# Performance work log

Measured on AMD Instinct MI355X. Metric: run time of the kernel, lower is better.

Reference implementation:

```python
import jax, jax.numpy as jnp
import numpy as np

DN = ('NCHW', 'OIHW', 'NCHW')

def _conv(x, w, b, pad):
    y = jax.lax.conv_general_dilated(x, w, (1, 1), pad, dimension_numbers=DN)
    return y + b[None, :, None, None]

def setup_inputs() -> dict:
    key = jax.random.key(0)
    ks = jax.random.split(key, 8)
    B, C, H, W = 8, 256, 64, 64
    C8 = C // 8
    return {
        'x': jax.random.normal(ks[0], (B, C, H, W), jnp.float32),
        'wq': jax.random.normal(ks[1], (C8, C, 1, 3), jnp.float32) * 0.02,
        'bq': jax.random.normal(ks[2], (C8,), jnp.float32) * 0.02,
        'wk': jax.random.normal(ks[3], (C8, C, 3, 1), jnp.float32) * 0.02,
        'bk': jax.random.normal(ks[4], (C8,), jnp.float32) * 0.02,
        'wv': jax.random.normal(ks[5], (C, C, 1, 1), jnp.float32) * 0.02,
        'bv': jax.random.normal(ks[6], (C,), jnp.float32) * 0.02,
        'gamma': jax.random.normal(ks[7], (1,), jnp.float32),
    }

def reference(x, wq, bq, wk, bk, wv, bv, gamma):
    B, C, H, W = x.shape
    N = H * W
    # q: (1,3) kernel, pad (0,1); k: (3,1) kernel, pad (1,0); v: 1x1
    q = _conv(x, wq, bq, [(0, 0), (1, 1)]).reshape(B, -1, N)  # B, C/8, N
    k = _conv(x, wk, bk, [(1, 1), (0, 0)]).reshape(B, -1, N)  # B, C/8, N
    v = _conv(x, wv, bv, [(0, 0), (0, 0)]).reshape(B, C, N)   # B, C, N
    affinity = jnp.einsum('bci,bcj->bij', q, k)               # B, N, N
    affinity = jax.nn.softmax(affinity, axis=-1)
    # weights = v @ affinity^T  ->  (B, C, N)
    weights = jnp.einsum('bcj,bij->bci', v, affinity).reshape(B, C, H, W)
    return gamma[0] * weights + x
```

## Files before the change

### kernel.cpp

```cpp
#include <hip/hip_runtime.h>
#include <math.h>

#define BB 8
#define CCH 256
#define C8 32
#define NN 4096
#define LOG2E 1.44269504f

typedef unsigned short us;
typedef __attribute__((ext_vector_type(8))) short bf16x8;
typedef __attribute__((ext_vector_type(4))) float f32x4;
typedef __attribute__((ext_vector_type(16))) float f32x16;

static __device__ __forceinline__ us f2bf(float f) {
  union { float f; unsigned u; } v; v.f = f;
  unsigned r = v.u + 0x7fffu + ((v.u >> 16) & 1u);
  return (us)(r >> 16);
}
static __device__ __forceinline__ us f2bf_rhu(float f) {
  return (us)((__float_as_uint(f) + 0x8000u) >> 16);
}
template <int CTRL>
static __device__ __forceinline__ float dpp_mv(float x) {
  return __int_as_float(
      __builtin_amdgcn_update_dpp(0, __float_as_int(x), CTRL, 0xF, 0xF, false));
}
static __device__ __forceinline__ float rowsum16(float t) {
  t += dpp_mv<0x121>(t);
  t += dpp_mv<0x122>(t);
  t += dpp_mv<0x124>(t);
  t += dpp_mv<0x128>(t);
  return t;
}

__global__ __launch_bounds__(256) void prep_kernel(
    const float* __restrict__ x, const float* __restrict__ wq,
    const float* __restrict__ wk, const float* __restrict__ wv,
    us* __restrict__ xT, us* __restrict__ wqc, us* __restrict__ wkc,
    us* __restrict__ wvb) {
  __shared__ __align__(16) us lt[64 * 68];
  int bid = blockIdx.x;
  int tid = threadIdx.x;
  if (bid < 2048) {
    int b = bid >> 8, cb = (bid >> 6) & 3, nb = bid & 63;
    const float* xb = x + (((size_t)(b * 256 + cb * 64)) << 12);
    int nl = tid & 63, ch = tid >> 6;
#pragma unroll
    for (int p = 0; p < 16; p++) {
      int c = p * 4 + ch;
      lt[nl * 68 + c] = f2bf(xb[((size_t)c << 12) + (nb * 64 + nl)]);
    }
    __syncthreads();
    us* xTb = xT + (((size_t)b << 12) + nb * 64) * 256 + cb * 64;
    int cw = tid & 7, nr0 = tid >> 3;
#pragma unroll
    for (int p2 = 0; p2 < 2; p2++) {
      int nr = p2 * 32 + nr0;
      uint2 lo = *(const uint2*)&lt[nr * 68 + cw * 8];
      uint2 hi = *(const uint2*)&lt[nr * 68 + cw * 8 + 4];
      *(uint4*)&xTb[(size_t)nr * 256 + cw * 8] = make_uint4(lo.x, lo.y, hi.x, hi.y);
    }
  } else {
    int idx = (bid - 2048) * 256 + tid;
    if (idx < 24576) {
      int oc = idx / 768, r = idx % 768, t = r >> 8, ic = r & 255;
      wqc[idx] = f2bf(wq[(oc * 256 + ic) * 3 + t] * LOG2E);
    } else if (idx < 49152) {
      int j = idx - 24576;
      int oc = j / 768, r = j % 768, t = r >> 8, ic = r & 255;
      wkc[j] = f2bf(wk[(oc * 256 + ic) * 3 + t]);
    } else if (idx < 114688) {
      int j = idx - 49152;
      wvb[j] = f2bf(wv[j]);
    }
  }
}

__global__ __launch_bounds__(256) void conv_kernel(
    const us* __restrict__ xT, const us* __restrict__ wqc,
    const us* __restrict__ wkc, const float* __restrict__ bq,
    const float* __restrict__ bk, const us* __restrict__ wvb,
    const float* __restrict__ bv, us* __restrict__ qT, us* __restrict__ kT,
    us* __restrict__ vblk) {
  int tid = threadIdx.x, lane = tid & 63, w = tid >> 6;
  int l15 = lane & 15, quad = lane >> 4;
  if (blockIdx.x < 512) {
    int bid = blockIdx.x;
    int b = bid & 7, rt = bid >> 3;
    int n0 = rt * 64, y = rt;
    bool isq = (w < 2);
    int m0 = (w & 1) * 16;
    const us* wc = isq ? wqc : wkc;
    const us* xTb = xT + (((size_t)b << 12) * 256);
    f32x4 acc[4];
#pragma unroll
    for (int nt = 0; nt < 4; nt++) acc[nt] = (f32x4){0.f, 0.f, 0.f, 0.f};
#pragma unroll
    for (int t = 0; t < 3; t++) {
      bool killT = (!isq) && ((t == 0 && y == 0) || (t == 2 && y == 63));
      if (!killT) {
        int dn = isq ? (t - 1) : (t - 1) * 64;
#pragma unroll
        for (int k8 = 0; k8 < 8; k8++) {
          int kloc = t * 256 + k8 * 32 + quad * 8;
          bf16x8 af = *(const bf16x8*)(wc + (size_t)(m0 + l15) * 768 + kloc);
          int ic = k8 * 32 + quad * 8;
#pragma unroll
          for (int nt = 0; nt < 4; nt++) {
            int nl = nt * 16 + l15;
            int ns = n0 + nl + dn;
            ns = ns < 0 ? 0 : (ns > 4095 ? 4095 : ns);
            bf16x8 bf = *(const bf16x8*)(xTb + (size_t)ns * 256 + ic);
            if (isq && ((t == 0 && nl == 0) || (t == 2 && nl == 63)))
              bf = (bf16x8){0, 0, 0, 0, 0, 0, 0, 0};
            acc[nt] = __builtin_amdgcn_mfma_f32_16x16x32_bf16(af, bf, acc[nt], 0, 0, 0);
          }
        }
      }
    }
    const float* bias = isq ? bq : bk;
    float bsc = isq ? LOG2E : 1.0f;
    us* outp = (isq ? qT : kT) + (((size_t)b << 12) * 32);
    float b0 = bias[m0 + quad * 4 + 0] * bsc;
    float b1 = bias[m0 + quad * 4 + 1] * bsc;
    float b2 = bias[m0 + quad * 4 + 2] * bsc;
    float b3 = bias[m0 + quad * 4 + 3] * bsc;
#pragma unroll
    for (int nt = 0; nt < 4; nt++) {
      int n = n0 + nt * 16 + l15;
      unsigned lo = (unsigned)f2bf(acc[nt][0] + b0) | ((unsigned)f2bf(acc[nt][1] + b1) << 16);
      unsigned hi = (unsigned)f2bf(acc[nt][2] + b2) | ((unsigned)f2bf(acc[nt][3] + b3) << 16);
      *(uint2*)(outp + (size_t)n * 32 + m0 + quad * 4) = make_uint2(lo, hi);
    }
  } else {
    int bid = blockIdx.x - 512;
    int b = bid & 7, nt0 = bid >> 3;
    int n0 = nt0 * 64;
    const us* xTb = xT + (((size_t)b << 12) * 256);
    f32x4 acc[4][4];
#pragma unroll
    for (int ct = 0; ct < 4; ct++)
#pragma unroll
      for (int nt = 0; nt < 4; nt++) acc[ct][nt] = (f32x4){0.f, 0.f, 0.f, 0.f};
#pragma unroll
    for (int kk = 0; kk < 8; kk++) {
      bf16x8 bfr[4];
#pragma unroll
      for (int nt = 0; nt < 4; nt++)
        bfr[nt] = *(const bf16x8*)(xTb + (size_t)(n0 + nt * 16 + l15) * 256 + kk * 32 + quad * 8);
#pragma unroll
      for (int ct = 0; ct < 4; ct++) {
        bf16x8 wf = *(const bf16x8*)(wvb + (size_t)(w * 64 + ct * 16 + l15) * 256 + kk * 32 + quad * 8);
#pragma unroll
        for (int nt = 0; nt < 4; nt++)
          acc[ct][nt] = __builtin_amdgcn_mfma_f32_16x16x32_bf16(bfr[nt], wf, acc[ct][nt], 0, 0, 0);
      }
    }
    us* vb = vblk + ((size_t)b << 20);
#pragma unroll
    for (int ct = 0; ct < 4; ct++) {
      int oc = w * 64 + ct * 16 + l15;
      float bvv = bv[oc];
#pragma unroll
      for (int nt = 0; nt < 4; nt++) {
        unsigned lo = (unsigned)f2bf(acc[ct][nt][0] + bvv) | ((unsigned)f2bf(acc[ct][nt][1] + bvv) << 16);
        unsigned hi = (unsigned)f2bf(acc[ct][nt][2] + bvv) | ((unsigned)f2bf(acc[ct][nt][3] + bvv) << 16);
        *(uint2*)(vb + ((size_t)((n0 >> 4) + nt) * 256 + oc) * 16 + quad * 4) = make_uint2(lo, hi);
      }
    }
  }
}

__global__ __launch_bounds__(512, 4) void attn_kernel(
    const float* __restrict__ x, const us* __restrict__ qT,
    const us* __restrict__ kT, const us* __restrict__ vblk,
    const float* __restrict__ gamma_p, float* __restrict__ out) {
  __shared__ __align__(16) us pb[2][64 * 136];
  __shared__ float lpart[2][64];

  int tid = threadIdx.x, lane = tid & 63, w = tid >> 6;
  int l15 = lane & 15, quad = lane >> 4;
  int l31 = lane & 31, h32 = lane >> 5;
  int tw = w & 3, jh = w >> 2;

  int bid = blockIdx.x;
  int b = bid & 7, i0 = (bid >> 3) * 64;

  const us* qTb = qT + (((size_t)b << 12) * 32);
  const us* kTb = kT + (((size_t)b << 12) * 32);
  const us* vbb = vblk + ((size_t)b << 20);

  bf16x8 qf = *(const bf16x8*)(qTb + (size_t)(i0 + tw * 16 + l15) * 32 + quad * 8);

  float lr[4] = {0.f, 0.f, 0.f, 0.f};
  f32x16 o[2];
#pragma unroll
  for (int it = 0; it < 2; it++)
#pragma unroll
    for (int rg = 0; rg < 16; rg++) o[it][rg] = 0.f;

  int bu = 0;
  for (int jt = 0; jt < 32; jt++) {
    int j0 = jt * 128;
    bf16x8 kf[4];
#pragma unroll
    for (int j2 = 0; j2 < 4; j2++)
      kf[j2] = *(const bf16x8*)(kTb + (size_t)(j0 + jh * 64 + j2 * 16 + l15) * 32 + quad * 8);
    bf16x8 vf[8];
#pragma unroll
    for (int ks = 0; ks < 8; ks++)
      vf[ks] = *(const bf16x8*)(vbb + ((size_t)((j0 >> 4) + ks) * 256 + w * 32 + l31) * 16 + h32 * 8);
    f32x4 s[4];
#pragma unroll
    for (int j2 = 0; j2 < 4; j2++)
      s[j2] = __builtin_amdgcn_mfma_f32_16x16x32_bf16(qf, kf[j2], (f32x4){0.f, 0.f, 0.f, 0.f}, 0, 0, 0);
    us* pw = &pb[bu][(tw * 16 + quad * 4) * 136 + jh * 64 + l15];
#pragma unroll
    for (int j2 = 0; j2 < 4; j2++)
#pragma unroll
      for (int r = 0; r < 4; r++) {
        float p = __builtin_amdgcn_exp2f(s[j2][r]);
        lr[r] += p;
        pw[r * 136 + j2 * 16] = f2bf_rhu(p);
      }
    __syncthreads();
#pragma unroll
    for (int ks = 0; ks < 8; ks++) {
      bf16x8 pf0 = *(const bf16x8*)&pb[bu][(size_t)l31 * 136 + ks * 16 + h32 * 8];
      bf16x8 pf1 = *(const bf16x8*)&pb[bu][(size_t)(32 + l31) * 136 + ks * 16 + h32 * 8];
      o[0] = __builtin_amdgcn_mfma_f32_32x32x16_bf16(vf[ks], pf0, o[0], 0, 0, 0);
      o[1] = __builtin_amdgcn_mfma_f32_32x32x16_bf16(vf[ks], pf1, o[1], 0, 0, 0);
    }
    bu ^= 1;
  }

  float ls[4];
#pragma unroll
  for (int r = 0; r < 4; r++) ls[r] = rowsum16(lr[r]);
  if (l15 == 0) {
#pragma unroll
    for (int r = 0; r < 4; r++) lpart[jh][tw * 16 + quad * 4 + r] = ls[r];
  }
  __syncthreads();
  float g = gamma_p[0];
  const float* xb = x + ((size_t)b << 20);
  float* ob = out + ((size_t)b << 20);
  float gl[2];
#pragma unroll
  for (int it = 0; it < 2; it++) {
    int i = it * 32 + l31;
    gl[it] = g / (lpart[0][i] + lpart[1][i]);
  }
#pragma unroll
  for (int it = 0; it < 2; it++) {
    int i = i0 + it * 32 + l31;
#pragma unroll
    for (int rg = 0; rg < 16; rg++) {
      int c = w * 32 + ((rg & 3) + 8 * (rg >> 2) + 4 * h32);
      size_t idx = ((size_t)c << 12) + i;
      ob[idx] = o[it][rg] * gl[it] + xb[idx];
    }
  }
}

extern "C" void kernel_launch(void* const* d_in, const int* in_sizes, int n_in,
                              void* d_out, int out_size, void* d_ws, size_t ws_size,
                              hipStream_t stream) {
  const float* x = (const float*)d_in[0];
  const float* wq = (const float*)d_in[1];
  const float* bq = (const float*)d_in[2];
  const float* wk = (const float*)d_in[3];
  const float* bk = (const float*)d_in[4];
  const float* wv = (const float*)d_in[5];
  const float* bv = (const float*)d_in[6];
  const float* gamma = (const float*)d_in[7];
  float* out = (float*)d_out;

  us* xT = (us*)d_ws;
  us* qT = xT + (size_t)8388608;
  us* kT = qT + (size_t)1048576;
  us* vblk = kT + (size_t)1048576;
  us* wqc = vblk + (size_t)8388608;
  us* wkc = wqc + (size_t)24576;
  us* wvb = wkc + (size_t)24576;

  prep_kernel<<<2496, 256, 0, stream>>>(x, wq, wk, wv, xT, wqc, wkc, wvb);
  conv_kernel<<<1024, 256, 0, stream>>>(xT, wqc, wkc, bq, bk, wvb, bv, qT, kT, vblk);
  attn_kernel<<<512, 512, 0, stream>>>(x, qT, kT, vblk, gamma, out);
}
```

Baseline: 236.7 us.

## Keep softmax probabilities in registers via permlane32 swap instead of LDS

Restructures the attention kernel so each wave computes a transposed 32x32 score tile (K·Q) with 32x32x16 MFMA. It then rearranges the exp'd probabilities between lane halves with permlane32_swap so they can feed the PV MFMA directly as the B operand. This removes the LDS probability buffer, the per-tile __syncthreads and the cross-wave rowsum reduction. Blocks shrink to 256 threads, each wave owning 32 queries by 128 channels, and the next K tile is prefetched. The cost is that each wave redoes QK for its half of the channels, so score compute is duplicated, and V loads per wave increase.

```diff
diff --git a/kernel.cpp b/kernel.cpp
--- a/kernel.cpp
+++ b/kernel.cpp
@@ -17,21 +17,29 @@
   unsigned r = v.u + 0x7fffu + ((v.u >> 16) & 1u);
   return (us)(r >> 16);
 }
-static __device__ __forceinline__ us f2bf_rhu(float f) {
-  return (us)((__float_as_uint(f) + 0x8000u) >> 16);
-}
-template <int CTRL>
-static __device__ __forceinline__ float dpp_mv(float x) {
-  return __int_as_float(
-      __builtin_amdgcn_update_dpp(0, __float_as_int(x), CTRL, 0xF, 0xF, false));
-}
-static __device__ __forceinline__ float rowsum16(float t) {
-  t += dpp_mv<0x121>(t);
-  t += dpp_mv<0x122>(t);
-  t += dpp_mv<0x124>(t);
-  t += dpp_mv<0x128>(t);
-  return t;
-}
+static __device__ __forceinline__ unsigned pk_rhu(float a, float b) {
+  unsigned ua = (__float_as_uint(a) + 0x8000u) >> 16;
+  unsigned ub = (__float_as_uint(b) + 0x8000u) & 0xffff0000u;
+  return ua | ub;
+}
+
+#if __has_builtin(__builtin_amdgcn_permlane32_swap)
+static __device__ __forceinline__ void lane32_swap(unsigned& hi, unsigned& lo) {
+  auto r = __builtin_amdgcn_permlane32_swap((int)hi, (int)lo, false, false);
+  hi = (unsigned)r[0];
+  lo = (unsigned)r[1];
+}
+#else
+static __device__ __forceinline__ void lane32_swap(unsigned& hi, unsigned& lo) {
+  unsigned ph = (unsigned)__shfl_xor((int)hi, 32);
+  unsigned pl = (unsigned)__shfl_xor((int)lo, 32);
+  bool up = (threadIdx.x & 32) != 0;
+  unsigned nh = up ? hi : pl;
+  unsigned nl = up ? ph : lo;
+  hi = nh;
+  lo = nl;
+}
+#endif
 
 __global__ __launch_bounds__(256) void prep_kernel(
     const float* __restrict__ x, const float* __restrict__ wq,
@@ -171,94 +179,91 @@
   }
 }
 
-__global__ __launch_bounds__(512, 4) void attn_kernel(
+__global__ __launch_bounds__(256, 2) void attn_kernel(
     const float* __restrict__ x, const us* __restrict__ qT,
     const us* __restrict__ kT, const us* __restrict__ vblk,
     const float* __restrict__ gamma_p, float* __restrict__ out) {
-  __shared__ __align__(16) us pb[2][64 * 136];
-  __shared__ float lpart[2][64];
-
-  int tid = threadIdx.x, lane = tid & 63, w = tid >> 6;
-  int l15 = lane & 15, quad = lane >> 4;
+  int tid = threadIdx.x, lane = tid & 63;
+  int w = tid >> 6;
   int l31 = lane & 31, h32 = lane >> 5;
-  int tw = w & 3, jh = w >> 2;
+  int chalf = w & 1, ihalf = w >> 1;
 
   int bid = blockIdx.x;
-  int b = bid & 7, i0 = (bid >> 3) * 64;
+  int b = bid & 7, i0 = (bid >> 3) * 64 + ihalf * 32;
+  int c0 = chalf * 128;
 
   const us* qTb = qT + (((size_t)b << 12) * 32);
   const us* kTb = kT + (((size_t)b << 12) * 32);
   const us* vbb = vblk + ((size_t)b << 20);
 
-  bf16x8 qf = *(const bf16x8*)(qTb + (size_t)(i0 + tw * 16 + l15) * 32 + quad * 8);
-
-  float lr[4] = {0.f, 0.f, 0.f, 0.f};
-  f32x16 o[2];
-#pragma unroll
-  for (int it = 0; it < 2; it++)
-#pragma unroll
-    for (int rg = 0; rg < 16; rg++) o[it][rg] = 0.f;
-
-  int bu = 0;
-  for (int jt = 0; jt < 32; jt++) {
-    int j0 = jt * 128;
-    bf16x8 kf[4];
-#pragma unroll
-    for (int j2 = 0; j2 < 4; j2++)
-      kf[j2] = *(const bf16x8*)(kTb + (size_t)(j0 + jh * 64 + j2 * 16 + l15) * 32 + quad * 8);
-    bf16x8 vf[8];
-#pragma unroll
-    for (int ks = 0; ks < 8; ks++)
-      vf[ks] = *(const bf16x8*)(vbb + ((size_t)((j0 >> 4) + ks) * 256 + w * 32 + l31) * 16 + h32 * 8);
-    f32x4 s[4];
-#pragma unroll
-    for (int j2 = 0; j2 < 4; j2++)
-      s[j2] = __builtin_amdgcn_mfma_f32_16x16x32_bf16(qf, kf[j2], (f32x4){0.f, 0.f, 0.f, 0.f}, 0, 0, 0);
-    us* pw = &pb[bu][(tw * 16 + quad * 4) * 136 + jh * 64 + l15];
-#pragma unroll
-    for (int j2 = 0; j2 < 4; j2++)
-#pragma unroll
-      for (int r = 0; r < 4; r++) {
-        float p = __builtin_amdgcn_exp2f(s[j2][r]);
-        lr[r] += p;
-        pw[r * 136 + j2 * 16] = f2bf_rhu(p);
-      }
-    __syncthreads();
-#pragma unroll
-    for (int ks = 0; ks < 8; ks++) {
-      bf16x8 pf0 = *(const bf16x8*)&pb[bu][(size_t)l31 * 136 + ks * 16 + h32 * 8];
-      bf16x8 pf1 = *(const bf16x8*)&pb[bu][(size_t)(32 + l31) * 136 + ks * 16 + h32 * 8];
-      o[0] = __builtin_amdgcn_mfma_f32_32x32x16_bf16(vf[ks], pf0, o[0], 0, 0, 0);
-      o[1] = __builtin_amdgcn_mfma_f32_32x32x16_bf16(vf[ks], pf1, o[1], 0, 0, 0);
-    }
-    bu ^= 1;
-  }
-
-  float ls[4];
-#pragma unroll
-  for (int r = 0; r < 4; r++) ls[r] = rowsum16(lr[r]);
-  if (l15 == 0) {
-#pragma unroll
-    for (int r = 0; r < 4; r++) lpart[jh][tw * 16 + quad * 4 + r] = ls[r];
-  }
-  __syncthreads();
-  float g = gamma_p[0];
+  bf16x8 qf0 = *(const bf16x8*)(qTb + (size_t)(i0 + l31) * 32 + h32 * 8);
+  bf16x8 qf1 = *(const bf16x8*)(qTb + (size_t)(i0 + l31) * 32 + 16 + h32 * 8);
+
+  float lsum = 0.f;
+  f32x16 o[4];
+#pragma unroll
+  for (int ct = 0; ct < 4; ct++)
+#pragma unroll
+    for (int rg = 0; rg < 16; rg++) o[ct][rg] = 0.f;
+
+  bf16x8 kf0 = *(const bf16x8*)(kTb + (size_t)l31 * 32 + h32 * 8);
+  bf16x8 kf1 = *(const bf16x8*)(kTb + (size_t)l31 * 32 + 16 + h32 * 8);
+
+  for (int jt = 0; jt < 128; jt++) {
+    int j0 = jt * 32;
+    bf16x8 vf[4][2];
+#pragma unroll
+    for (int ct = 0; ct < 4; ct++)
+#pragma unroll
+      for (int win = 0; win < 2; win++)
+        vf[ct][win] = *(const bf16x8*)(vbb + ((size_t)((j0 >> 4) + win) * 256 + c0 + ct * 32 + l31) * 16 + h32 * 8);
+    f32x16 s;
+#pragma unroll
+    for (int rg = 0; rg < 16; rg++) s[rg] = 0.f;
+    s = __builtin_amdgcn_mfma_f32_32x32x16_bf16(kf0, qf0, s, 0, 0, 0);
+    s = __builtin_amdgcn_mfma_f32_32x32x16_bf16(kf1, qf1, s, 0, 0, 0);
+    {
+      int jn = (jt < 127) ? (j0 + 32) : 0;
+      kf0 = *(const bf16x8*)(kTb + (size_t)(jn + l31) * 32 + h32 * 8);
+      kf1 = *(const bf16x8*)(kTb + (size_t)(jn + l31) * 32 + 16 + h32 * 8);
+    }
+    unsigned pk[8];
+#pragma unroll
+    for (int t = 0; t < 8; t++) {
+      float p0 = __builtin_amdgcn_exp2f(s[2 * t]);
+      float p1 = __builtin_amdgcn_exp2f(s[2 * t + 1]);
+      lsum += p0 + p1;
+      pk[t] = pk_rhu(p0, p1);
+    }
+    lane32_swap(pk[2], pk[0]);
+    lane32_swap(pk[3], pk[1]);
+    lane32_swap(pk[6], pk[4]);
+    lane32_swap(pk[7], pk[5]);
+    union {
+      unsigned u[4];
+      bf16x8 v;
+    } w0, w1;
+    w0.u[0] = pk[0]; w0.u[1] = pk[1]; w0.u[2] = pk[2]; w0.u[3] = pk[3];
+    w1.u[0] = pk[4]; w1.u[1] = pk[5]; w1.u[2] = pk[6]; w1.u[3] = pk[7];
+#pragma unroll
+    for (int ct = 0; ct < 4; ct++) {
+      o[ct] = __builtin_amdgcn_mfma_f32_32x32x16_bf16(vf[ct][0], w0.v, o[ct], 0, 0, 0);
+      o[ct] = __builtin_amdgcn_mfma_f32_32x32x16_bf16(vf[ct][1], w1.v, o[ct], 0, 0, 0);
+    }
+  }
+
+  float lfull = lsum + __shfl_xor(lsum, 32);
+  float gl = gamma_p[0] / lfull;
   const float* xb = x + ((size_t)b << 20);
   float* ob = out + ((size_t)b << 20);
-  float gl[2];
-#pragma unroll
-  for (int it = 0; it < 2; it++) {
-    int i = it * 32 + l31;
-    gl[it] = g / (lpart[0][i] + lpart[1][i]);
-  }
-#pragma unroll
-  for (int it = 0; it < 2; it++) {
-    int i = i0 + it * 32 + l31;
+  int i = i0 + l31;
+#pragma unroll
+  for (int ct = 0; ct < 4; ct++) {
 #pragma unroll
     for (int rg = 0; rg < 16; rg++) {
-      int c = w * 32 + ((rg & 3) + 8 * (rg >> 2) + 4 * h32);
+      int c = c0 + ct * 32 + ((rg & 3) + 8 * (rg >> 2) + 4 * h32);
       size_t idx = ((size_t)c << 12) + i;
-      ob[idx] = o[it][rg] * gl[it] + xb[idx];
+      ob[idx] = o[ct][rg] * gl + xb[idx];
     }
   }
 }
@@ -286,5 +291,5 @@
 
   prep_kernel<<<2496, 256, 0, stream>>>(x, wq, wk, wv, xT, wqc, wkc, wvb);
   conv_kernel<<<1024, 256, 0, stream>>>(xT, wqc, wkc, bq, bk, wvb, bv, qT, kT, vblk);
-  attn_kernel<<<512, 512, 0, stream>>>(x, qT, kT, vblk, gamma, out);
-}
+  attn_kernel<<<512, 256, 0, stream>>>(x, qT, kT, vblk, gamma, out);
+}
```

Result: slower. 255.4 us (+7.9%).
